# Performance work log

Hardware: AMD Instinct MI355X
Metric: run time of the kernel (lower is better)

Reference implementation:

```python
import jax, jax.numpy as jnp
import numpy as np

QUERY_DIM = 1024
KEY_DIM = 1024
NUM_HEADS = 16
HEAD_DIM = QUERY_DIM // NUM_HEADS


def setup_inputs() -> dict:
    key = jax.random.key(0)
    ks = jax.random.split(key, 12)
    B, Sq, Sk = 2, 1024, 4096

    def xavier(k, fan_in, fan_out):
        limit = np.sqrt(6.0 / (fan_in + fan_out))
        return jax.random.uniform(k, (fan_in, fan_out), jnp.float32, -limit, limit)

    return {
        "query": jax.random.normal(ks[0], (B, Sq, QUERY_DIM), jnp.float32),
        "key": jax.random.normal(ks[1], (B, Sk, KEY_DIM), jnp.float32),
        "value": jax.random.normal(ks[2], (B, Sk, KEY_DIM), jnp.float32),
        "key_mask": jax.random.randint(ks[3], (B, Sk), 0, 2, jnp.int32),
        # projection weights stored as [in, out] for x @ W
        "Wq": xavier(ks[4], QUERY_DIM, NUM_HEADS * HEAD_DIM),
        "bq": jnp.zeros((NUM_HEADS * HEAD_DIM,), jnp.float32),
        "Wk": xavier(ks[5], KEY_DIM, NUM_HEADS * HEAD_DIM),
        "bk": jnp.zeros((NUM_HEADS * HEAD_DIM,), jnp.float32),
        "Wv": xavier(ks[6], KEY_DIM, NUM_HEADS * HEAD_DIM),
        "bv": jnp.zeros((NUM_HEADS * HEAD_DIM,), jnp.float32),
        "Wo": xavier(ks[7], NUM_HEADS * HEAD_DIM, QUERY_DIM),
        "bo": jnp.zeros((QUERY_DIM,), jnp.float32),
    }


def reference(query, key, value, key_mask, Wq, bq, Wk, bk, Wv, bv, Wo, bo):
    B, Sq, _ = query.shape
    Sk = key.shape[1]
    H, D = NUM_HEADS, HEAD_DIM
    scale = 1.0 / np.sqrt(D)

    q = (query @ Wq + bq).reshape(B, Sq, H, D)   # [B,Sq,H,D]
    k = (key @ Wk + bk).reshape(B, Sk, H, D)     # [B,Sk,H,D]
    v = (value @ Wv + bv).reshape(B, Sk, H, D)

    # scores: [B,H,Sq,Sk]
    scores = jnp.einsum("bqhd,bkhd->bhqk", q, k) * scale
    mask = (key_mask == 0)[:, None, None, :]  # [B,1,1,Sk]
    scores = jnp.where(mask, jnp.float32(-1e9), scores)
    probs = jax.nn.softmax(scores, axis=-1)
    # dropout is identity at eval (p effectively 0)
    ctx = jnp.einsum("bhqk,bkhd->bqhd", probs, v).reshape(B, Sq, H * D)
    return ctx @ Wo + bo
```

## Files before the change

kernel.cpp:

```cpp
#include <hip/hip_runtime.h>
#include <stdint.h>

#define NH 16
#define HD 64
#define SQ 1024
#define SK 4096
#define DM 1024
#define MQ 2048
#define MK 8192
#define MTOT 18432

typedef short s16x8 __attribute__((ext_vector_type(8)));
typedef short s16x4 __attribute__((ext_vector_type(4)));
typedef float f32x4 __attribute__((ext_vector_type(4)));

#define GLOAD_LDS16(g, l) __builtin_amdgcn_global_load_lds( \
    (const __attribute__((address_space(1))) void*)(g), \
    (__attribute__((address_space(3))) void*)(l), 16, 0, 0)

__device__ __forceinline__ short f2bf(float f) {
  union { float f; uint32_t u; } v; v.f = f;
  uint32_t r = (v.u + 0x7FFFu + ((v.u >> 16) & 1u)) >> 16;
  return (short)(uint16_t)r;
}
__device__ __forceinline__ short f2bf_rz(float f) {
  union { float f; uint32_t u; } v; v.f = f;
  return (short)(uint16_t)(v.u >> 16);
}

__global__ void cvt_kernel(const float* __restrict__ src, short* __restrict__ dst, int n8) {
  int stride = gridDim.x * blockDim.x;
  for (int i = blockIdx.x * blockDim.x + threadIdx.x; i < n8; i += stride) {
    const float4* s4 = (const float4*)src + 2 * (size_t)i;
    float4 a = s4[0], b = s4[1];
    s16x8 o;
    o[0] = f2bf(a.x); o[1] = f2bf(a.y); o[2] = f2bf(a.z); o[3] = f2bf(a.w);
    o[4] = f2bf(b.x); o[5] = f2bf(b.y); o[6] = f2bf(b.z); o[7] = f2bf(b.w);
    *((s16x8*)dst + i) = o;
  }
}

__global__ void maskf_kernel(const int* __restrict__ km, float* __restrict__ madd_g) {
  int i = blockIdx.x * 256 + threadIdx.x;
  if (i < 2 * SK) madd_g[i] = km[i] ? -8.0f : -1e9f;
}

__global__ void twkernel(const float* __restrict__ W, short* __restrict__ Wt) {
  __shared__ __align__(16) short t[64][65];
  int lx = threadIdx.x & 63, ly = threadIdx.x >> 6;
  int c0 = (blockIdx.x & 15) * 64, r0 = (blockIdx.x >> 4) * 64;
  #pragma unroll
  for (int i = ly; i < 64; i += 4) t[i][lx] = f2bf(W[(size_t)(r0 + i) * DM + c0 + lx]);
  __syncthreads();
  #pragma unroll
  for (int i = ly; i < 64; i += 4) Wt[(size_t)(c0 + i) * DM + r0 + lx] = t[lx][i];
}

__global__ __launch_bounds__(256) void proj_gemm(
    const short* __restrict__ Acat,
    const short* __restrict__ Wqt, const short* __restrict__ Wkt, const short* __restrict__ Wvt,
    const float* __restrict__ bq, const float* __restrict__ bk, const float* __restrict__ bv,
    short* __restrict__ Qp, short* __restrict__ Kp, short* __restrict__ Vp)
{
  __shared__ __align__(16) short As[128 * 64];
  __shared__ __align__(16) short Bs[128 * 64];
  int tid = threadIdx.x, lane = tid & 63, wid = tid >> 6;
  int bm = blockIdx.x >> 3, bn = blockIdx.x & 7;
  int m0 = bm * 128, n0 = bn * 128;
  int seg = (m0 < MQ) ? 0 : (m0 < MQ + MK) ? 1 : 2;
  const short* Wt = (seg == 0) ? Wqt : (seg == 1) ? Wkt : Wvt;
  const float* bias = (seg == 0) ? bq : (seg == 1) ? bk : bv;

  int rs = tid >> 3;
  int cb8 = (tid & 7) * 8;
  int wr = wid >> 1, wc = wid & 1;
  int l15 = lane & 15, g = lane >> 4;

  f32x4 acc[4][4] = {};

  const short* gA = Acat + (size_t)(m0 + rs) * DM + cb8;
  const short* gB = Wt + (size_t)(n0 + rs) * DM + cb8;
  char* lA = (char*)As + tid * 16;
  char* lB = (char*)Bs + tid * 16;

  for (int kt = 0; kt < 16; ++kt) {
    int k0 = kt * 64;
    __syncthreads();
    GLOAD_LDS16(gA + k0,            lA);
    GLOAD_LDS16(gA + 32 * DM + k0,  lA + 4096);
    GLOAD_LDS16(gA + 64 * DM + k0,  lA + 8192);
    GLOAD_LDS16(gA + 96 * DM + k0,  lA + 12288);
    GLOAD_LDS16(gB + k0,            lB);
    GLOAD_LDS16(gB + 32 * DM + k0,  lB + 4096);
    GLOAD_LDS16(gB + 64 * DM + k0,  lB + 8192);
    GLOAD_LDS16(gB + 96 * DM + k0,  lB + 12288);
    __syncthreads();
    #pragma unroll
    for (int kk = 0; kk < 2; ++kk) {
      s16x8 af[4], bfr[4];
      #pragma unroll
      for (int mi = 0; mi < 4; ++mi)
        af[mi] = *(const s16x8*)((const char*)As + (wr * 64 + mi * 16 + l15) * 128 + kk * 64 + g * 16);
      #pragma unroll
      for (int ni = 0; ni < 4; ++ni)
        bfr[ni] = *(const s16x8*)((const char*)Bs + (wc * 64 + ni * 16 + l15) * 128 + kk * 64 + g * 16);
      #pragma unroll
      for (int mi = 0; mi < 4; ++mi)
        #pragma unroll
        for (int ni = 0; ni < 4; ++ni)
          acc[mi][ni] = __builtin_amdgcn_mfma_f32_16x16x32_bf16(af[mi], bfr[ni], acc[mi][ni], 0, 0, 0);
    }
  }

  __syncthreads();

  if (seg == 2) {
    short* tw = (short*)As + wid * 288;
    int vbase = m0 - (MQ + MK) + wr * 64;
    #pragma unroll
    for (int mi = 0; mi < 4; ++mi) {
      int vr = vbase + mi * 16 + l15;
      int bb2 = vr >> 12, sk = vr & 4095;
      #pragma unroll
      for (int ni = 0; ni < 4; ++ni) {
        int col = n0 + wc * 64 + ni * 16;
        int h = col >> 6, d0 = col & 63;
        float bb = bias[col + l15];
        #pragma unroll
        for (int r = 0; r < 4; ++r)
          tw[(g * 4 + r) * 18 + l15] = f2bf(acc[mi][ni][r] + bb);
        #pragma unroll
        for (int j = 0; j < 4; ++j) {
          int dl = g * 4 + j;
          Vp[((size_t)(bb2 * NH + h) * HD + d0 + dl) * SK + sk] = tw[l15 * 18 + dl];
        }
      }
    }
  } else {
    char* tw2 = (char*)As + wid * 2048;
    int hh = (n0 + wc * 64) >> 6;
    short* outp = (seg == 0) ? Qp : Kp;
    int sdim = (seg == 0) ? SQ : SK;
    int rbase = (seg == 0) ? m0 : m0 - MQ;
    int rmask = (seg == 0) ? 1023 : 4095;
    int rshift = (seg == 0) ? 10 : 12;
    #pragma unroll
    for (int mi = 0; mi < 4; ++mi) {
      #pragma unroll
      for (int ni = 0; ni < 4; ++ni) {
        float bb = bias[n0 + wc * 64 + ni * 16 + l15];
        #pragma unroll
        for (int r = 0; r < 4; ++r) {
          int rw = g * 4 + r;
          *(short*)(tw2 + rw * 128 + (((ni * 16 + l15) * 2) ^ ((rw & 7) << 4))) =
              f2bf(acc[mi][ni][r] + bb);
        }
      }
      asm volatile("s_waitcnt lgkmcnt(0)" ::: "memory");
      #pragma unroll
      for (int pp = 0; pp < 2; ++pp) {
        int lr = pp * 8 + (lane >> 3);
        int ce = (lane & 7) * 8;
        s16x8 v8 = *(const s16x8*)(tw2 + lr * 128 + ((ce * 2) ^ ((lr & 7) << 4)));
        int row = rbase + wr * 64 + mi * 16 + lr;
        int bI = row >> rshift, s = row & rmask;
        *(s16x8*)(outp + ((size_t)(bI * NH + hh) * sdim + s) * HD + ce) = v8;
      }
      asm volatile("s_waitcnt lgkmcnt(0)" ::: "memory");
    }
  }
}

__global__ __launch_bounds__(256) void attn_kernel(
    const short* __restrict__ Qp, const short* __restrict__ Kp, const short* __restrict__ Vp,
    const float* __restrict__ madd_g, float* __restrict__ po, float* __restrict__ pl)
{
  __shared__ __align__(16) short Ks[2][64 * 64];
  __shared__ __align__(16) short Vs[2][64 * 64];
  __shared__ __align__(16) short Ps[4][16 * 64];

  int tid = threadIdx.x, lane = tid & 63, wid = tid >> 6;
  int sub = blockIdx.x & 63, qt = blockIdx.x >> 6;
  int bh = sub >> 1, half = sub & 1;
  int b = bh >> 4;
  const short* Qb = Qp + (size_t)bh * SQ * HD;
  const short* Kb = Kp + (size_t)bh * SK * HD + (size_t)half * 2048 * HD;
  const short* Vb = Vp + (size_t)bh * HD * SK + half * 2048;
  const float* mab = madd_g + b * SK + half * 2048;

  int l15 = lane & 15, g = lane >> 4, lh8 = g * 8;
  int q0 = qt * 64 + wid * 16;
  int swz = (l15 & 7) << 4;

  s16x8 aq[2];
  aq[0] = *(const s16x8*)(Qb + (size_t)(q0 + l15) * HD + lh8);
  aq[1] = *(const s16x8*)(Qb + (size_t)(q0 + l15) * HD + 32 + lh8);

  s16x8 ones;
  #pragma unroll
  for (int j = 0; j < 8; ++j) ones[j] = (short)0x3F80;

  f32x4 o[4] = {};
  f32x4 ol = {};

  int srow = tid >> 3, scEl = (tid & 7) * 8;
  int wsoff = srow * 128 + ((scEl * 2) ^ ((srow & 7) << 4));

  s16x8 rk0, rk1, rv0, rv1;
#define ALOADS(t) { \
    rk0 = *(const s16x8*)(Kb + (size_t)((t) * 64 + srow) * HD + scEl); \
    rk1 = *(const s16x8*)(Kb + (size_t)((t) * 64 + srow + 32) * HD + scEl); \
    rv0 = *(const s16x8*)(Vb + (size_t)srow * SK + (t) * 64 + scEl); \
    rv1 = *(const s16x8*)(Vb + (size_t)(srow + 32) * SK + (t) * 64 + scEl); }
#define STAGE(bi) { \
    char* kb_ = (char*)Ks[bi]; char* vb_ = (char*)Vs[bi]; \
    *(s16x8*)(kb_ + wsoff) = rk0; *(s16x8*)(kb_ + wsoff + 4096) = rk1; \
    *(s16x8*)(vb_ + wsoff) = rv0; *(s16x8*)(vb_ + wsoff + 4096) = rv1; }

  ALOADS(0); STAGE(0); ALOADS(1);
  __syncthreads();

  const float sscale = 0.18033688f;
  for (int t = 0; t < 32; ++t) {
    int cur = t & 1;
    if (t < 31) STAGE(cur ^ 1);
    if (t < 30) ALOADS(t + 2);
    const char* KsB = (const char*)Ks[cur];
    const char* VsB = (const char*)Vs[cur];

    f32x4 sc[4] = {};
    __builtin_amdgcn_s_setprio(1);
    #pragma unroll
    for (int ni = 0; ni < 4; ++ni) {
      #pragma unroll
      for (int ks = 0; ks < 2; ++ks) {
        s16x8 kf = *(const s16x8*)(KsB + (ni * 16 + l15) * 128 + ((ks * 64 + g * 16) ^ swz));
        sc[ni] = __builtin_amdgcn_mfma_f32_16x16x32_bf16(aq[ks], kf, sc[ni], 0, 0, 0);
      }
    }
    __builtin_amdgcn_s_setprio(0);

    char* PsW = (char*)&Ps[wid][0];
    #pragma unroll
    for (int ni = 0; ni < 4; ++ni) {
      float ma = mab[t * 64 + ni * 16 + l15];
      #pragma unroll
      for (int r = 0; r < 4; ++r) {
        float p = exp2f(sc[ni][r] * sscale + ma);
        int prow = g * 4 + r;
        *(short*)(PsW + prow * 128 + (((ni * 16 + l15) * 2) ^ ((prow & 7) << 4))) = f2bf_rz(p);
      }
    }
    asm volatile("s_waitcnt lgkmcnt(0)" ::: "memory");

    __builtin_amdgcn_s_setprio(1);
    #pragma unroll
    for (int ks2 = 0; ks2 < 2; ++ks2) {
      s16x8 pa = *(const s16x8*)(PsW + l15 * 128 + ((ks2 * 64 + g * 16) ^ swz));
      #pragma unroll
      for (int nd = 0; nd < 4; ++nd) {
        s16x8 vf = *(const s16x8*)(VsB + (nd * 16 + l15) * 128 + ((ks2 * 64 + g * 16) ^ swz));
        o[nd] = __builtin_amdgcn_mfma_f32_16x16x32_bf16(pa, vf, o[nd], 0, 0, 0);
      }
      ol = __builtin_amdgcn_mfma_f32_16x16x32_bf16(pa, ones, ol, 0, 0, 0);
    }
    __builtin_amdgcn_s_setprio(0);
    __syncthreads();
  }
#undef ALOADS
#undef STAGE

  float* poB = po + (size_t)blockIdx.x * 4096;
  #pragma unroll
  for (int nd = 0; nd < 4; ++nd) {
    #pragma unroll
    for (int r = 0; r < 4; ++r) {
      int ql = wid * 16 + g * 4 + r;
      poB[ql * 64 + nd * 16 + l15] = o[nd][r];
    }
  }
  if (l15 == 0) {
    #pragma unroll
    for (int r = 0; r < 4; ++r)
      pl[(size_t)blockIdx.x * 64 + wid * 16 + g * 4 + r] = ol[r];
  }
}

__global__ __launch_bounds__(256) void combine_kernel(
    const float* __restrict__ po, const float* __restrict__ pl, short* __restrict__ ctx)
{
  int tg = blockIdx.x * 256 + threadIdx.x;
  int d4 = (tg & 15) * 4;
  int idx = tg >> 4;
  int bh = idx >> 10, qrow = idx & 1023;
  int qt = qrow >> 6, ql = qrow & 63;
  int pid0 = qt * 64 + bh * 2;
  const float4 a = *(const float4*)(po + (size_t)pid0 * 4096 + ql * 64 + d4);
  const float4 c = *(const float4*)(po + (size_t)(pid0 + 1) * 4096 + ql * 64 + d4);
  float rl = 1.0f / (pl[(size_t)pid0 * 64 + ql] + pl[(size_t)(pid0 + 1) * 64 + ql]);
  s16x4 outv;
  outv[0] = f2bf((a.x + c.x) * rl);
  outv[1] = f2bf((a.y + c.y) * rl);
  outv[2] = f2bf((a.z + c.z) * rl);
  outv[3] = f2bf((a.w + c.w) * rl);
  int b = bh >> 4, h = bh & 15;
  *(s16x4*)(ctx + ((size_t)(b * SQ + qrow)) * DM + h * HD + d4) = outv;
}

__global__ __launch_bounds__(256) void out_gemm(
    const short* __restrict__ Actx, const short* __restrict__ Wot,
    const float* __restrict__ bo, float* __restrict__ out)
{
  __shared__ __align__(16) short As[128 * 64];
  __shared__ __align__(16) short Bs[128 * 64];
  int tid = threadIdx.x, lane = tid & 63, wid = tid >> 6;
  int bm = blockIdx.x >> 3, bn = blockIdx.x & 7;
  int m0 = bm * 128, n0 = bn * 128;

  int rs = tid >> 3;
  int cb8 = (tid & 7) * 8;
  int wr = wid >> 1, wc = wid & 1;
  int l15 = lane & 15, g = lane >> 4;

  f32x4 acc[4][4] = {};

  const short* gA = Actx + (size_t)(m0 + rs) * DM + cb8;
  const short* gB = Wot + (size_t)(n0 + rs) * DM + cb8;
  char* lA = (char*)As + tid * 16;
  char* lB = (char*)Bs + tid * 16;

  for (int kt = 0; kt < 16; ++kt) {
    int k0 = kt * 64;
    __syncthreads();
    GLOAD_LDS16(gA + k0,            lA);
    GLOAD_LDS16(gA + 32 * DM + k0,  lA + 4096);
    GLOAD_LDS16(gA + 64 * DM + k0,  lA + 8192);
    GLOAD_LDS16(gA + 96 * DM + k0,  lA + 12288);
    GLOAD_LDS16(gB + k0,            lB);
    GLOAD_LDS16(gB + 32 * DM + k0,  lB + 4096);
    GLOAD_LDS16(gB + 64 * DM + k0,  lB + 8192);
    GLOAD_LDS16(gB + 96 * DM + k0,  lB + 12288);
    __syncthreads();
    #pragma unroll
    for (int kk = 0; kk < 2; ++kk) {
      s16x8 af[4], bfr[4];
      #pragma unroll
      for (int mi = 0; mi < 4; ++mi)
        af[mi] = *(const s16x8*)((const char*)As + (wr * 64 + mi * 16 + l15) * 128 + kk * 64 + g * 16);
      #pragma unroll
      for (int ni = 0; ni < 4; ++ni)
        bfr[ni] = *(const s16x8*)((const char*)Bs + (wc * 64 + ni * 16 + l15) * 128 + kk * 64 + g * 16);
      #pragma unroll
      for (int mi = 0; mi < 4; ++mi)
        #pragma unroll
        for (int ni = 0; ni < 4; ++ni)
          acc[mi][ni] = __builtin_amdgcn_mfma_f32_16x16x32_bf16(af[mi], bfr[ni], acc[mi][ni], 0, 0, 0);
    }
  }

  #pragma unroll
  for (int mi = 0; mi < 4; ++mi) {
    #pragma unroll
    for (int ni = 0; ni < 4; ++ni) {
      int col = n0 + wc * 64 + ni * 16 + l15;
      float bb = bo[col];
      #pragma unroll
      for (int r = 0; r < 4; ++r) {
        int row = m0 + wr * 64 + mi * 16 + g * 4 + r;
        out[(size_t)row * DM + col] = acc[mi][ni][r] + bb;
      }
    }
  }
}

extern "C" void kernel_launch(void* const* d_in, const int* in_sizes, int n_in,
                              void* d_out, int out_size, void* d_ws, size_t ws_size,
                              hipStream_t stream) {
  const float* query = (const float*)d_in[0];
  const float* key   = (const float*)d_in[1];
  const float* value = (const float*)d_in[2];
  const int*   kmask = (const int*)d_in[3];
  const float* Wq = (const float*)d_in[4];
  const float* bq = (const float*)d_in[5];
  const float* Wk = (const float*)d_in[6];
  const float* bk = (const float*)d_in[7];
  const float* Wv = (const float*)d_in[8];
  const float* bv = (const float*)d_in[9];
  const float* Wo = (const float*)d_in[10];
  const float* bo = (const float*)d_in[11];
  float* out = (float*)d_out;

  char* ws = (char*)d_ws;
  short* Acat = (short*)ws;
  short* Wqt  = (short*)(ws + (size_t)37748736);
  short* Wkt  = Wqt + 1048576;
  short* Wvt  = Wkt + 1048576;
  short* Wot  = Wvt + 1048576;
  short* Qp   = Wot + 1048576;
  short* Kp   = Qp + 2097152;
  short* Vp   = Kp + 8388608;
  short* ctx  = Vp + 8388608;
  float* madd_g = (float*)(ctx + 2097152);

  float* po = (float*)Acat;
  float* pl = po + (size_t)1024 * 4096;

  short* qbf = Acat;
  short* kbf = Acat + 2097152;
  short* vbf = Acat + 2097152 + 8388608;

  cvt_kernel<<<1024, 256, 0, stream>>>(query, qbf, 2097152 / 8);
  cvt_kernel<<<2048, 256, 0, stream>>>(key,   kbf, 8388608 / 8);
  cvt_kernel<<<2048, 256, 0, stream>>>(value, vbf, 8388608 / 8);
  maskf_kernel<<<32, 256, 0, stream>>>(kmask, madd_g);
  twkernel<<<256, 256, 0, stream>>>(Wq, Wqt);
  twkernel<<<256, 256, 0, stream>>>(Wk, Wkt);
  twkernel<<<256, 256, 0, stream>>>(Wv, Wvt);
  twkernel<<<256, 256, 0, stream>>>(Wo, Wot);
  proj_gemm<<<1152, 256, 0, stream>>>(Acat, Wqt, Wkt, Wvt, bq, bk, bv, Qp, Kp, Vp);
  attn_kernel<<<1024, 256, 0, stream>>>(Qp, Kp, Vp, madd_g, po, pl);
  combine_kernel<<<2048, 256, 0, stream>>>(po, pl, ctx);
  out_gemm<<<128, 256, 0, stream>>>(ctx, Wot, bo, out);
}
```

Measured before the change: 357.2 us.

## Drop split-K attention, fuse combine, merge prep kernels, pack mask as bits

The attention kernel now processes the full 4096-key range per block (512 blocks instead of 1024) and normalizes and writes bf16 context directly, removing the partial-output buffers and the combine kernel. The three input conversion kernels and the mask kernel are merged into one prep kernel that packs the key mask into bitwords, and the four weight transposes are merged into one launch. K staging is single-buffered with an extra barrier per tile to free LDS for a mask cache. The aim is fewer launches and less intermediate global traffic, at the cost of half the attention grid parallelism and one more sync per iteration.

```diff
diff --git a/kernel.cpp b/kernel.cpp
--- a/kernel.cpp
+++ b/kernel.cpp
@@ -28,27 +28,43 @@
   return (short)(uint16_t)(v.u >> 16);
 }
 
-__global__ void cvt_kernel(const float* __restrict__ src, short* __restrict__ dst, int n8) {
-  int stride = gridDim.x * blockDim.x;
-  for (int i = blockIdx.x * blockDim.x + threadIdx.x; i < n8; i += stride) {
-    const float4* s4 = (const float4*)src + 2 * (size_t)i;
+__global__ void prep_kernel(const float* __restrict__ q, const float* __restrict__ k,
+                            const float* __restrict__ v, const int* __restrict__ km,
+                            short* __restrict__ qbf, short* __restrict__ kbf,
+                            short* __restrict__ vbf, uint32_t* __restrict__ mbits) {
+  int gid = blockIdx.x * 256 + threadIdx.x;
+  if (gid < 256) {
+    const int* kmw = km + gid * 32;
+    uint32_t bits = 0;
+    #pragma unroll
+    for (int j = 0; j < 32; ++j) bits |= (kmw[j] ? 1u : 0u) << j;
+    mbits[gid] = bits;
+  }
+  int stride = gridDim.x * 256;
+  for (int i = gid; i < 2359296; i += stride) {
+    const float* src; short* dst; int off;
+    if (i < 262144)       { src = q; dst = qbf; off = i; }
+    else if (i < 1310720) { src = k; dst = kbf; off = i - 262144; }
+    else                  { src = v; dst = vbf; off = i - 1310720; }
+    const float4* s4 = (const float4*)src + 2 * (size_t)off;
     float4 a = s4[0], b = s4[1];
     s16x8 o;
     o[0] = f2bf(a.x); o[1] = f2bf(a.y); o[2] = f2bf(a.z); o[3] = f2bf(a.w);
     o[4] = f2bf(b.x); o[5] = f2bf(b.y); o[6] = f2bf(b.z); o[7] = f2bf(b.w);
-    *((s16x8*)dst + i) = o;
-  }
-}
-
-__global__ void maskf_kernel(const int* __restrict__ km, float* __restrict__ madd_g) {
-  int i = blockIdx.x * 256 + threadIdx.x;
-  if (i < 2 * SK) madd_g[i] = km[i] ? -8.0f : -1e9f;
-}
-
-__global__ void twkernel(const float* __restrict__ W, short* __restrict__ Wt) {
+    *((s16x8*)dst + off) = o;
+  }
+}
+
+__global__ void twall_kernel(const float* __restrict__ Wq, const float* __restrict__ Wk,
+                             const float* __restrict__ Wv, const float* __restrict__ Wo,
+                             short* __restrict__ Wqt, short* __restrict__ Wkt,
+                             short* __restrict__ Wvt, short* __restrict__ Wot) {
   __shared__ __align__(16) short t[64][65];
+  int wsel = blockIdx.x >> 8, bid = blockIdx.x & 255;
+  const float* W = (wsel == 0) ? Wq : (wsel == 1) ? Wk : (wsel == 2) ? Wv : Wo;
+  short* Wt = (wsel == 0) ? Wqt : (wsel == 1) ? Wkt : (wsel == 2) ? Wvt : Wot;
   int lx = threadIdx.x & 63, ly = threadIdx.x >> 6;
-  int c0 = (blockIdx.x & 15) * 64, r0 = (blockIdx.x >> 4) * 64;
+  int c0 = (bid & 15) * 64, r0 = (bid >> 4) * 64;
   #pragma unroll
   for (int i = ly; i < 64; i += 4) t[i][lx] = f2bf(W[(size_t)(r0 + i) * DM + c0 + lx]);
   __syncthreads();
@@ -173,20 +189,21 @@
 
 __global__ __launch_bounds__(256) void attn_kernel(
     const short* __restrict__ Qp, const short* __restrict__ Kp, const short* __restrict__ Vp,
-    const float* __restrict__ madd_g, float* __restrict__ po, float* __restrict__ pl)
+    const uint32_t* __restrict__ mbits_g, short* __restrict__ ctx)
 {
-  __shared__ __align__(16) short Ks[2][64 * 64];
+  __shared__ __align__(16) short Ks[64 * 64];
   __shared__ __align__(16) short Vs[2][64 * 64];
   __shared__ __align__(16) short Ps[4][16 * 64];
+  __shared__ uint32_t mb[128];
 
   int tid = threadIdx.x, lane = tid & 63, wid = tid >> 6;
-  int sub = blockIdx.x & 63, qt = blockIdx.x >> 6;
-  int bh = sub >> 1, half = sub & 1;
-  int b = bh >> 4;
+  int bh = blockIdx.x & 31, qt = blockIdx.x >> 5;
+  int b = bh >> 4, h = bh & 15;
   const short* Qb = Qp + (size_t)bh * SQ * HD;
-  const short* Kb = Kp + (size_t)bh * SK * HD + (size_t)half * 2048 * HD;
-  const short* Vb = Vp + (size_t)bh * HD * SK + half * 2048;
-  const float* mab = madd_g + b * SK + half * 2048;
+  const short* Kb = Kp + (size_t)bh * SK * HD;
+  const short* Vb = Vp + (size_t)bh * HD * SK;
+
+  if (tid < 128) mb[tid] = mbits_g[b * 128 + tid];
 
   int l15 = lane & 15, g = lane >> 4, lh8 = g * 8;
   int q0 = qt * 64 + wid * 16;
@@ -212,21 +229,20 @@
     rk1 = *(const s16x8*)(Kb + (size_t)((t) * 64 + srow + 32) * HD + scEl); \
     rv0 = *(const s16x8*)(Vb + (size_t)srow * SK + (t) * 64 + scEl); \
     rv1 = *(const s16x8*)(Vb + (size_t)(srow + 32) * SK + (t) * 64 + scEl); }
-#define STAGE(bi) { \
-    char* kb_ = (char*)Ks[bi]; char* vb_ = (char*)Vs[bi]; \
-    *(s16x8*)(kb_ + wsoff) = rk0; *(s16x8*)(kb_ + wsoff + 4096) = rk1; \
+#define STAGE_K() { \
+    *(s16x8*)((char*)Ks + wsoff) = rk0; *(s16x8*)((char*)Ks + wsoff + 4096) = rk1; }
+#define STAGE_V(bi) { \
+    char* vb_ = (char*)Vs[bi]; \
     *(s16x8*)(vb_ + wsoff) = rv0; *(s16x8*)(vb_ + wsoff + 4096) = rv1; }
 
-  ALOADS(0); STAGE(0); ALOADS(1);
+  ALOADS(0); STAGE_K(); STAGE_V(0);
+  ALOADS(1);
   __syncthreads();
 
   const float sscale = 0.18033688f;
-  for (int t = 0; t < 32; ++t) {
+  for (int t = 0; t < 64; ++t) {
     int cur = t & 1;
-    if (t < 31) STAGE(cur ^ 1);
-    if (t < 30) ALOADS(t + 2);
-    const char* KsB = (const char*)Ks[cur];
-    const char* VsB = (const char*)Vs[cur];
+    if (t < 63) STAGE_V(cur ^ 1);
 
     f32x4 sc[4] = {};
     __builtin_amdgcn_s_setprio(1);
@@ -234,16 +250,22 @@
     for (int ni = 0; ni < 4; ++ni) {
       #pragma unroll
       for (int ks = 0; ks < 2; ++ks) {
-        s16x8 kf = *(const s16x8*)(KsB + (ni * 16 + l15) * 128 + ((ks * 64 + g * 16) ^ swz));
+        s16x8 kf = *(const s16x8*)((const char*)Ks + (ni * 16 + l15) * 128 + ((ks * 64 + g * 16) ^ swz));
         sc[ni] = __builtin_amdgcn_mfma_f32_16x16x32_bf16(aq[ks], kf, sc[ni], 0, 0, 0);
       }
     }
     __builtin_amdgcn_s_setprio(0);
-
+    __syncthreads();
+
+    if (t < 63) STAGE_K();
+    if (t < 62) ALOADS(t + 2);
+
+    uint32_t w0 = mb[2 * t], w1 = mb[2 * t + 1];
     char* PsW = (char*)&Ps[wid][0];
     #pragma unroll
     for (int ni = 0; ni < 4; ++ni) {
-      float ma = mab[t * 64 + ni * 16 + l15];
+      uint32_t w = (ni < 2) ? w0 : w1;
+      float ma = ((w >> ((ni & 1) * 16 + l15)) & 1u) ? -8.0f : -1e9f;
       #pragma unroll
       for (int r = 0; r < 4; ++r) {
         float p = exp2f(sc[ni][r] * sscale + ma);
@@ -253,6 +275,7 @@
     }
     asm volatile("s_waitcnt lgkmcnt(0)" ::: "memory");
 
+    const char* VsB = (const char*)Vs[cur];
     __builtin_amdgcn_s_setprio(1);
     #pragma unroll
     for (int ks2 = 0; ks2 < 2; ++ks2) {
@@ -268,43 +291,19 @@
     __syncthreads();
   }
 #undef ALOADS
-#undef STAGE
-
-  float* poB = po + (size_t)blockIdx.x * 4096;
+#undef STAGE_K
+#undef STAGE_V
+
   #pragma unroll
   for (int nd = 0; nd < 4; ++nd) {
     #pragma unroll
     for (int r = 0; r < 4; ++r) {
-      int ql = wid * 16 + g * 4 + r;
-      poB[ql * 64 + nd * 16 + l15] = o[nd][r];
-    }
-  }
-  if (l15 == 0) {
-    #pragma unroll
-    for (int r = 0; r < 4; ++r)
-      pl[(size_t)blockIdx.x * 64 + wid * 16 + g * 4 + r] = ol[r];
-  }
-}
-
-__global__ __launch_bounds__(256) void combine_kernel(
-    const float* __restrict__ po, const float* __restrict__ pl, short* __restrict__ ctx)
-{
-  int tg = blockIdx.x * 256 + threadIdx.x;
-  int d4 = (tg & 15) * 4;
-  int idx = tg >> 4;
-  int bh = idx >> 10, qrow = idx & 1023;
-  int qt = qrow >> 6, ql = qrow & 63;
-  int pid0 = qt * 64 + bh * 2;
-  const float4 a = *(const float4*)(po + (size_t)pid0 * 4096 + ql * 64 + d4);
-  const float4 c = *(const float4*)(po + (size_t)(pid0 + 1) * 4096 + ql * 64 + d4);
-  float rl = 1.0f / (pl[(size_t)pid0 * 64 + ql] + pl[(size_t)(pid0 + 1) * 64 + ql]);
-  s16x4 outv;
-  outv[0] = f2bf((a.x + c.x) * rl);
-  outv[1] = f2bf((a.y + c.y) * rl);
-  outv[2] = f2bf((a.z + c.z) * rl);
-  outv[3] = f2bf((a.w + c.w) * rl);
-  int b = bh >> 4, h = bh & 15;
-  *(s16x4*)(ctx + ((size_t)(b * SQ + qrow)) * DM + h * HD + d4) = outv;
+      int q = q0 + g * 4 + r;
+      int d = nd * 16 + l15;
+      float val = o[nd][r] / ol[r];
+      ctx[((size_t)(b * SQ + q)) * DM + h * HD + d] = f2bf(val);
+    }
+  }
 }
 
 __global__ __launch_bounds__(256) void out_gemm(
@@ -400,25 +399,15 @@
   short* Kp   = Qp + 2097152;
   short* Vp   = Kp + 8388608;
   short* ctx  = Vp + 8388608;
-  float* madd_g = (float*)(ctx + 2097152);
-
-  float* po = (float*)Acat;
-  float* pl = po + (size_t)1024 * 4096;
+  uint32_t* mbits = (uint32_t*)(ctx + 2097152);
 
   short* qbf = Acat;
   short* kbf = Acat + 2097152;
   short* vbf = Acat + 2097152 + 8388608;
 
-  cvt_kernel<<<1024, 256, 0, stream>>>(query, qbf, 2097152 / 8);
-  cvt_kernel<<<2048, 256, 0, stream>>>(key,   kbf, 8388608 / 8);
-  cvt_kernel<<<2048, 256, 0, stream>>>(value, vbf, 8388608 / 8);
-  maskf_kernel<<<32, 256, 0, stream>>>(kmask, madd_g);
-  twkernel<<<256, 256, 0, stream>>>(Wq, Wqt);
-  twkernel<<<256, 256, 0, stream>>>(Wk, Wkt);
-  twkernel<<<256, 256, 0, stream>>>(Wv, Wvt);
-  twkernel<<<256, 256, 0, stream>>>(Wo, Wot);
+  prep_kernel<<<2048, 256, 0, stream>>>(query, key, value, kmask, qbf, kbf, vbf, mbits);
+  twall_kernel<<<1024, 256, 0, stream>>>(Wq, Wk, Wv, Wo, Wqt, Wkt, Wvt, Wot);
   proj_gemm<<<1152, 256, 0, stream>>>(Acat, Wqt, Wkt, Wvt, bq, bk, bv, Qp, Kp, Vp);
-  attn_kernel<<<1024, 256, 0, stream>>>(Qp, Kp, Vp, madd_g, po, pl);
-  combine_kernel<<<2048, 256, 0, stream>>>(po, pl, ctx);
+  attn_kernel<<<512, 256, 0, stream>>>(Qp, Kp, Vp, mbits, ctx);
   out_gemm<<<128, 256, 0, stream>>>(ctx, Wot, bo, out);
 }
```

Measured after the change: 325.4 us. 8.9% less time.
